# Performance work log

Hardware: AMD Instinct MI355X
Metric: run time of the kernel (lower is better)

## Reference

```python
import jax, jax.numpy as jnp
import numpy as np
import math

N_HEAD = 16

def setup_inputs() -> dict:
    key = jax.random.key(0)
    ks = jax.random.split(key, 5)
    B, T, C = 4, 2048, 2048
    s = 1.0 / math.sqrt(C)
    return {
        "x": jax.random.normal(ks[0], (B, T, C), jnp.float32),
        "w_attn": jax.random.normal(ks[1], (C, 3 * C), jnp.float32) * s,
        "b_attn": jax.random.normal(ks[2], (3 * C,), jnp.float32) * 0.01,
        "w_proj": jax.random.normal(ks[3], (C, C), jnp.float32) * s,
        "b_proj": jax.random.normal(ks[4], (C,), jnp.float32) * 0.01,
    }

def reference(x, w_attn, b_attn, w_proj, b_proj):
    B, T, C = x.shape
    H = N_HEAD
    D = C // H
    # fused QKV projection: [B,T,3C] -> [3,B,H,T,D]
    qkv = (x @ w_attn + b_attn).reshape(B, T, 3, H, D).transpose(2, 0, 3, 1, 4)
    q, k, v = qkv[0], qkv[1], qkv[2]
    scale = 1.0 / math.sqrt(D)
    scores = jnp.einsum("bhqd,bhkd->bhqk", q, k) * scale  # [B,H,T,T]
    causal = jnp.tril(jnp.ones((T, T), dtype=bool))
    neg = jnp.finfo(scores.dtype).min
    scores = jnp.where(causal, scores, neg)
    attn = jax.nn.softmax(scores, axis=-1)
    y = jnp.einsum("bhqk,bhkd->bhqd", attn, v)  # [B,H,T,D]
    y = y.transpose(0, 2, 1, 3).reshape(B, T, C)
    return y @ w_proj + b_proj
```

## Files before the change

kernel.cpp:

```cpp
#include <hip/hip_runtime.h>
#include <hip/hip_bf16.h>
#include <stdint.h>

typedef unsigned short u16;
typedef __bf16 bf16x8 __attribute__((ext_vector_type(8)));
typedef unsigned short u16x8 __attribute__((ext_vector_type(8)));
typedef float f32x4 __attribute__((ext_vector_type(4)));

__device__ __forceinline__ float bf2f(u16 u){ union{float f; unsigned i;} v; v.i = ((unsigned)u)<<16; return v.f; }
__device__ __forceinline__ u16 f2bf(float f){ union{float f; unsigned i;} v; v.f=f; unsigned r = v.i + 0x7FFFu + ((v.i>>16)&1u); return (u16)(r>>16); }

__device__ __forceinline__ void async16(const void* g, void* l){
  __builtin_amdgcn_global_load_lds((const __attribute__((address_space(1))) void*)g,
                                   (__attribute__((address_space(3))) void*)l, 16, 0, 0);
}

__global__ __launch_bounds__(256) void cvt_f2b(const float* __restrict__ src, u16* __restrict__ dst, int n)
{
  int i = (blockIdx.x * 256 + threadIdx.x) * 4;
  if (i < n) {
    float4 v = *(const float4*)&src[i];
    ushort4 o;
    o.x = f2bf(v.x); o.y = f2bf(v.y); o.z = f2bf(v.z); o.w = f2bf(v.w);
    *(ushort4*)&dst[i] = o;
  }
}

__global__ __launch_bounds__(256) void transpose2d_f2b(const float* __restrict__ src, u16* __restrict__ dst,
                                                       int src_rows, int src_cols)
{
  __shared__ u16 tile[64][72];
  const int r0 = blockIdx.y << 6, c0 = blockIdx.x << 6;
  const int t = threadIdx.x;
  #pragma unroll
  for (int i=0;i<4;i++){
    int slot = t + (i<<8);
    int r = slot >> 4, cv = (slot & 15) << 2;
    float4 v = *(const float4*)&src[(size_t)(r0+r)*src_cols + c0 + cv];
    tile[r][cv+0] = f2bf(v.x); tile[r][cv+1] = f2bf(v.y);
    tile[r][cv+2] = f2bf(v.z); tile[r][cv+3] = f2bf(v.w);
  }
  __syncthreads();
  #pragma unroll
  for (int i=0;i<2;i++){
    int slot = t + (i<<8);
    int cr = slot >> 3, rv = (slot & 7) << 3;
    u16x8 v;
    #pragma unroll
    for (int e=0;e<8;e++) v[e] = tile[rv+e][cr];
    *(u16x8*)&dst[(size_t)(c0+cr)*src_rows + r0 + rv] = v;
  }
}

__global__ __launch_bounds__(256) void transpose_v(const u16* __restrict__ qkv, u16* __restrict__ vt)
{
  __shared__ u16 tile[64][72];
  const int bh = blockIdx.z;
  const int b = bh >> 4, h = bh & 15;
  const u16* src = qkv + (size_t)b*2048*6144 + 4096 + h*128;
  u16* dst = vt + (size_t)bh*128*2048;
  const int t0 = blockIdx.y << 6, d0 = blockIdx.x << 6;
  const int t = threadIdx.x;
  #pragma unroll
  for (int i=0;i<2;i++){
    int slot = t + (i<<8);
    int r = slot >> 3, cv = (slot & 7) << 3;
    *(u16x8*)&tile[r][cv] = *(const u16x8*)&src[(size_t)(t0+r)*6144 + d0 + cv];
  }
  __syncthreads();
  #pragma unroll
  for (int i=0;i<2;i++){
    int slot = t + (i<<8);
    int cr = slot >> 3, rv = (slot & 7) << 3;
    u16x8 v;
    #pragma unroll
    for (int e=0;e<8;e++) v[e] = tile[rv+e][cr];
    *(u16x8*)&dst[(size_t)(d0+cr)*2048 + t0 + rv] = v;
  }
}

template<int F32OUT>
__global__ __launch_bounds__(512, 2) void gemm8p(const u16* __restrict__ A, const u16* __restrict__ Bt,
                                                 const float* __restrict__ bias, void* __restrict__ Cv,
                                                 int M, int N, int K, int mtiles)
{
  __shared__ u16 lsA[2][2][256*32];
  __shared__ u16 lsB[2][2][256*32];
  const int tid = threadIdx.x;
  const int w = tid >> 6, lane = tid & 63;
  const int wm = w >> 2, wn = w & 3;
  const int lo = lane & 15, hi = lane >> 4;

  const int nwg = gridDim.x;
  const int bid = blockIdx.x;
  const int swz = (bid & 7) * (nwg >> 3) + (bid >> 3);
  const int mt = swz % mtiles, nt = swz / mtiles;
  const int m0 = mt << 8, n0 = nt << 8;
  const int NT = K >> 6, NI = NT >> 1;

  const int s0 = tid, s1 = tid + 512;
  const size_t off0 = (size_t)(s0>>2)*K + (size_t)((((s0&3) ^ ((s0>>3)&3))) << 3);
  const size_t off1 = (size_t)(s1>>2)*K + (size_t)((((s1&3) ^ ((s1>>3)&3))) << 3);
  const u16* Asrc = A + (size_t)m0*K;
  const u16* Bsrc = Bt + (size_t)n0*K;

  f32x4 acc[8][4];
  f32x4 z = {0.f,0.f,0.f,0.f};
  #pragma unroll
  for (int i=0;i<8;i++)
    #pragma unroll
    for (int j=0;j<4;j++) acc[i][j] = z;

  bf16x8 bfr[4];

#define SLOT(T, KH, AP, BP) do { \
    const u16* as_ = Asrc + (T)*64 + (KH)*32; \
    const u16* bs_ = Bsrc + (T)*64 + (KH)*32; \
    async16(as_ + off0, &(AP)[s0*8]); \
    async16(as_ + off1, &(AP)[s1*8]); \
    async16(bs_ + off0, &(BP)[s0*8]); \
    async16(bs_ + off1, &(BP)[s1*8]); \
  } while(0)

#define LOADB(BUF, KS) do { \
    _Pragma("unroll") \
    for (int nf=0; nf<4; ++nf){ \
      int row_ = wn*64 + nf*16 + lo; \
      bfr[nf] = *(const bf16x8*)&lsB[BUF][KS][row_*32 + ((hi ^ ((row_>>1) & 3)) << 3)]; \
    } } while(0)

#define VM8 asm volatile("s_waitcnt vmcnt(8)" ::: "memory")
#define VM4 asm volatile("s_waitcnt vmcnt(4)" ::: "memory")
#define VM0 asm volatile("s_waitcnt vmcnt(0)" ::: "memory")
#define VMN do{}while(0)

#define PH(BUF, KS, Q, LB, WAIT, ...) do { \
    bf16x8 a_[4]; \
    _Pragma("unroll") \
    for (int mf=0; mf<4; ++mf){ \
      int row_ = wm*128 + Q*64 + mf*16 + lo; \
      a_[mf] = *(const bf16x8*)&lsA[BUF][KS][row_*32 + ((hi ^ ((row_>>1) & 3)) << 3)]; \
    } \
    if (LB) LOADB(BUF, KS); \
    __VA_ARGS__; \
    __builtin_amdgcn_s_barrier(); \
    __builtin_amdgcn_s_setprio(1); \
    _Pragma("unroll") \
    for (int mf=0; mf<4; ++mf) \
      _Pragma("unroll") \
      for (int nf=0; nf<4; ++nf) \
        acc[Q*4+mf][nf] = __builtin_amdgcn_mfma_f32_16x16x32_bf16(a_[mf], bfr[nf], acc[Q*4+mf][nf], 0,0,0); \
    __builtin_amdgcn_s_setprio(0); \
    WAIT; \
    __builtin_amdgcn_s_barrier(); \
    __builtin_amdgcn_sched_barrier(0); \
  } while(0)

  SLOT(0, 0, lsA[0][0], lsB[0][0]);
  SLOT(0, 1, lsA[0][1], lsB[0][1]);
  SLOT(1, 0, lsA[1][0], lsB[1][0]);
  VM8;
  __builtin_amdgcn_s_barrier();
  __builtin_amdgcn_sched_barrier(0);

  #pragma unroll 1
  for (int i = 0; i < NI-1; ++i){
    const int t0 = 2*i;
    PH(0,0,0, 1, VMN, SLOT(t0+1,1, lsA[1][1], lsB[1][1]));
    PH(0,0,1, 0, VM8, VMN);
    PH(0,1,0, 1, VMN, SLOT(t0+2,0, lsA[0][0], lsB[0][0]));
    PH(0,1,1, 0, VM8, VMN);
    PH(1,0,0, 1, VMN, SLOT(t0+2,1, lsA[0][1], lsB[0][1]));
    PH(1,0,1, 0, VM8, VMN);
    PH(1,1,0, 1, VMN, SLOT(t0+3,0, lsA[1][0], lsB[1][0]));
    PH(1,1,1, 0, VM8, VMN);
  }
  PH(0,0,0, 1, VMN, SLOT(NT-1,1, lsA[1][1], lsB[1][1]));
  PH(0,0,1, 0, VM8, VMN);
  PH(0,1,0, 1, VMN, VMN);
  PH(0,1,1, 0, VM4, VMN);
  PH(1,0,0, 1, VMN, VMN);
  PH(1,0,1, 0, VM0, VMN);
  PH(1,1,0, 1, VMN, VMN);
  PH(1,1,1, 0, VMN, VMN);

#undef PH
#undef SLOT
#undef LOADB

  float bv[4];
  #pragma unroll
  for (int nf=0;nf<4;nf++) bv[nf] = bias[n0 + wn*64 + nf*16 + lo];
  #pragma unroll
  for (int am=0;am<8;am++){
    int row = m0 + wm*128 + am*16 + hi*4;
    #pragma unroll
    for (int nf=0;nf<4;nf++){
      int col = n0 + wn*64 + nf*16 + lo;
      #pragma unroll
      for (int r=0;r<4;r++){
        float vv = acc[am][nf][r] + bv[nf];
        if (F32OUT) ((float*)Cv)[(size_t)(row+r)*N + col] = vv;
        else        ((u16*)Cv)[(size_t)(row+r)*N + col] = f2bf(vv);
      }
    }
  }
}

__global__ __launch_bounds__(512, 4) void attn_fwd(const u16* __restrict__ qkv, const u16* __restrict__ vt,
                                                   u16* __restrict__ y)
{
  __shared__ u16 kb[2][64*128];
  __shared__ u16 vb[2][128*64];
  __shared__ u16 plds[8][16*64];
  const int bh = blockIdx.y;
  const int b = bh >> 4, h = bh & 15;
  const int pair = blockIdx.x;
  const int tid = threadIdx.x;
  const int w = tid >> 6, lane = tid & 63;
  const int lo = lane & 15, hi = lane >> 4;

  const u16* Qb = qkv + (size_t)b*2048*6144 + h*128;
  const u16* Kb = Qb + 2048;
  const u16* Vb = vt + (size_t)bh*128*2048;
  u16* pw = &plds[w][0];
  const float sc = 0.08838834764831845f * 1.4426950408889634f;
  f32x4 z = {0.f,0.f,0.f,0.f};

  #pragma unroll 1
  for (int seg = 0; seg < 2; ++seg){
    const int qt = seg ? pair : 15 - pair;
    const int qw = qt*128 + w*16;
    const int nt = qt*2 + 2;

    bf16x8 qf[4];
    #pragma unroll
    for (int kd=0;kd<4;kd++)
      qf[kd] = *(const bf16x8*)&Qb[(size_t)(qw + lo)*6144 + kd*32 + hi*8];

    f32x4 o[8];
    #pragma unroll
    for (int dj=0;dj<8;dj++) o[dj] = z;
    float mx[4], lsum[4];
    #pragma unroll
    for (int r=0;r<4;r++){ mx[r] = -3.0e38f; lsum[r] = 0.f; }

    #pragma unroll
    for (int i=0;i<2;i++){
      int slot = i*512 + tid;
      int kr = slot >> 4;
      int kc = ((slot & 15) << 4) ^ ((kr & 7) << 4);
      async16(Kb + (size_t)kr*6144 + (kc >> 1), &kb[0][(size_t)(i*512 + w*64)*8]);
      int vr = slot >> 3;
      int vc = ((slot & 7) << 4) ^ ((vr & 7) << 4);
      async16(Vb + (size_t)vr*2048 + (vc >> 1), &vb[0][(size_t)(i*512 + w*64)*8]);
    }
    __syncthreads();

    #pragma unroll 1
    for (int it = 0; it < nt; ++it){
      const int k0 = it*64;
      if (it + 1 < nt){
        const int kn = (it+1)*64;
        u16* kdst = kb[(it+1)&1];
        u16* vdst = vb[(it+1)&1];
        #pragma unroll
        for (int i=0;i<2;i++){
          int slot = i*512 + tid;
          int kr = slot >> 4;
          int kc = ((slot & 15) << 4) ^ ((kr & 7) << 4);
          async16(Kb + (size_t)(kn + kr)*6144 + (kc >> 1), &kdst[(size_t)(i*512 + w*64)*8]);
          int vr = slot >> 3;
          int vc = ((slot & 7) << 4) ^ ((vr & 7) << 4);
          async16(Vb + (size_t)vr*2048 + kn + (vc >> 1), &vdst[(size_t)(i*512 + w*64)*8]);
        }
      }
      if (k0 <= qw + 15){
        const u16* kcur = kb[it&1];
        const u16* vcur = vb[it&1];
        f32x4 s[4];
        #pragma unroll
        for (int t=0;t<4;t++) s[t] = z;
        __builtin_amdgcn_s_setprio(1);
        #pragma unroll
        for (int t=0;t<4;t++){
          #pragma unroll
          for (int kd=0;kd<4;kd++){
            int row = t*16 + lo;
            int cb = (kd*64 + hi*16) ^ ((lo & 7) << 4);
            bf16x8 kk = *(const bf16x8*)&kcur[row*128 + (cb >> 1)];
            s[t] = __builtin_amdgcn_mfma_f32_16x16x32_bf16(qf[kd], kk, s[t], 0,0,0);
          }
        }
        __builtin_amdgcn_s_setprio(0);

        if (k0 + 63 > qw) {
          #pragma unroll
          for (int t=0;t<4;t++)
            #pragma unroll
            for (int r=0;r<4;r++){
              int q = qw + hi*4 + r;
              int k = k0 + t*16 + lo;
              if (k > q) s[t][r] = -3.0e38f;
            }
        }
        #pragma unroll
        for (int r=0;r<4;r++){
          float tm = fmaxf(fmaxf(s[0][r], s[1][r]), fmaxf(s[2][r], s[3][r]));
          tm = fmaxf(tm, __shfl_xor(tm, 1));
          tm = fmaxf(tm, __shfl_xor(tm, 2));
          tm = fmaxf(tm, __shfl_xor(tm, 4));
          tm = fmaxf(tm, __shfl_xor(tm, 8));
          tm *= sc;
          float mn = fmaxf(mx[r], tm);
          float al = exp2f(mx[r] - mn);
          mx[r] = mn;
          float p0 = exp2f(fmaf(s[0][r], sc, -mn));
          float p1 = exp2f(fmaf(s[1][r], sc, -mn));
          float p2 = exp2f(fmaf(s[2][r], sc, -mn));
          float p3 = exp2f(fmaf(s[3][r], sc, -mn));
          float sum = (p0 + p1) + (p2 + p3);
          sum += __shfl_xor(sum, 1);
          sum += __shfl_xor(sum, 2);
          sum += __shfl_xor(sum, 4);
          sum += __shfl_xor(sum, 8);
          lsum[r] = lsum[r]*al + sum;
          #pragma unroll
          for (int dj=0;dj<8;dj++) o[dj][r] *= al;
          int row = hi*4 + r;
          int sw = (row & 7) << 4;
          u16* prow = pw + row*64;
          prow[((     lo*2) ^ sw) >> 1] = f2bf(p0);
          prow[((32 + lo*2) ^ sw) >> 1] = f2bf(p1);
          prow[((64 + lo*2) ^ sw) >> 1] = f2bf(p2);
          prow[((96 + lo*2) ^ sw) >> 1] = f2bf(p3);
        }

        bf16x8 pa[2];
        #pragma unroll
        for (int kf=0;kf<2;kf++)
          pa[kf] = *(const bf16x8*)&pw[(lo*128 + ((kf*64 + hi*16) ^ ((lo & 7) << 4))) >> 1];
        __builtin_amdgcn_s_setprio(1);
        #pragma unroll
        for (int dj=0;dj<8;dj++){
          int row = dj*16 + lo;
          int cb0 = (hi*16)      ^ ((lo & 7) << 4);
          int cb1 = (64 + hi*16) ^ ((lo & 7) << 4);
          bf16x8 vv0 = *(const bf16x8*)&vcur[row*64 + (cb0 >> 1)];
          bf16x8 vv1 = *(const bf16x8*)&vcur[row*64 + (cb1 >> 1)];
          o[dj] = __builtin_amdgcn_mfma_f32_16x16x32_bf16(pa[0], vv0, o[dj], 0,0,0);
          o[dj] = __builtin_amdgcn_mfma_f32_16x16x32_bf16(pa[1], vv1, o[dj], 0,0,0);
        }
        __builtin_amdgcn_s_setprio(0);
      }
      __syncthreads();
    }

    #pragma unroll
    for (int r=0;r<4;r++){
      float inv = 1.0f / lsum[r];
      size_t row = (size_t)(b*2048 + qw + hi*4 + r);
      #pragma unroll
      for (int dj=0;dj<8;dj++)
        y[row*2048 + h*128 + dj*16 + lo] = f2bf(o[dj][r] * inv);
    }
    __syncthreads();
  }
}

extern "C" void kernel_launch(void* const* d_in, const int* in_sizes, int n_in,
                              void* d_out, int out_size, void* d_ws, size_t ws_size,
                              hipStream_t stream) {
  (void)in_sizes; (void)n_in; (void)out_size; (void)ws_size;
  const float* x      = (const float*)d_in[0];
  const float* w_attn = (const float*)d_in[1];
  const float* b_attn = (const float*)d_in[2];
  const float* w_proj = (const float*)d_in[3];
  const float* b_proj = (const float*)d_in[4];
  float* out = (float*)d_out;

  char* ws = (char*)d_ws;
  u16* xbf = (u16*)(ws);
  u16* wT  = (u16*)(ws + 33554432);
  u16* pT  = (u16*)(ws + 58720256);
  u16* qkv = (u16*)(ws + 67108864);
  u16* vt  = (u16*)(ws + 167772160);
  u16* y   = xbf;

  cvt_f2b<<<16384, 256, 0, stream>>>(x, xbf, 8192*2048);
  transpose2d_f2b<<<dim3(96,32), 256, 0, stream>>>(w_attn, wT, 2048, 6144);
  transpose2d_f2b<<<dim3(32,32), 256, 0, stream>>>(w_proj, pT, 2048, 2048);
  gemm8p<0><<<768, 512, 0, stream>>>(xbf, wT, b_attn, qkv, 8192, 6144, 2048, 32);
  transpose_v<<<dim3(2,32,64), 256, 0, stream>>>(qkv, vt);
  attn_fwd<<<dim3(8,64), 512, 0, stream>>>(qkv, vt, y);
  gemm8p<1><<<256, 512, 0, stream>>>(y, pT, b_proj, out, 8192, 2048, 2048, 32);
}
```

Measured before the change: 527.1 us.

## Software-pipeline LDS fragment reads one phase ahead of MFMA in GEMM

Restructures the GEMM main loop so LDS reads for the next phase's A and B fragments are issued before the current phase's MFMAs. Double-buffered register sets (aE/aO, bX/bY) and lgkmcnt waits replace the per-phase read-then-compute sequence, and one of the two barriers per phase is removed. The goal is to hide LDS read latency behind matrix-core work, at the cost of more VGPRs and more fragile waitcnt ordering.

Result: faster. 506.9 us (-3.8%).

```diff
diff --git a/kernel.cpp b/kernel.cpp
--- a/kernel.cpp
+++ b/kernel.cpp
@@ -111,7 +111,7 @@
     #pragma unroll
     for (int j=0;j<4;j++) acc[i][j] = z;
 
-  bf16x8 bfr[4];
+  bf16x8 aE[4], aO[4], bX[4], bY[4];
 
 #define SLOT(T, KH, AP, BP) do { \
     const u16* as_ = Asrc + (T)*64 + (KH)*32; \
@@ -122,39 +122,37 @@
     async16(bs_ + off1, &(BP)[s1*8]); \
   } while(0)
 
-#define LOADB(BUF, KS) do { \
+#define RDA(SET, BUF, KS, Q) do { \
+    _Pragma("unroll") \
+    for (int mf=0; mf<4; ++mf){ \
+      int row_ = wm*128 + (Q)*64 + mf*16 + lo; \
+      SET[mf] = *(const bf16x8*)&lsA[BUF][KS][row_*32 + ((hi ^ ((row_>>1) & 3)) << 3)]; \
+    } } while(0)
+
+#define RDB(SET, BUF, KS) do { \
     _Pragma("unroll") \
     for (int nf=0; nf<4; ++nf){ \
       int row_ = wn*64 + nf*16 + lo; \
-      bfr[nf] = *(const bf16x8*)&lsB[BUF][KS][row_*32 + ((hi ^ ((row_>>1) & 3)) << 3)]; \
+      SET[nf] = *(const bf16x8*)&lsB[BUF][KS][row_*32 + ((hi ^ ((row_>>1) & 3)) << 3)]; \
     } } while(0)
 
-#define VM8 asm volatile("s_waitcnt vmcnt(8)" ::: "memory")
-#define VM4 asm volatile("s_waitcnt vmcnt(4)" ::: "memory")
-#define VM0 asm volatile("s_waitcnt vmcnt(0)" ::: "memory")
-#define VMN do{}while(0)
-
-#define PH(BUF, KS, Q, LB, WAIT, ...) do { \
-    bf16x8 a_[4]; \
-    _Pragma("unroll") \
-    for (int mf=0; mf<4; ++mf){ \
-      int row_ = wm*128 + Q*64 + mf*16 + lo; \
-      a_[mf] = *(const bf16x8*)&lsA[BUF][KS][row_*32 + ((hi ^ ((row_>>1) & 3)) << 3)]; \
-    } \
-    if (LB) LOADB(BUF, KS); \
-    __VA_ARGS__; \
-    __builtin_amdgcn_s_barrier(); \
+#define MM(Q, AS, BS) do { \
     __builtin_amdgcn_s_setprio(1); \
     _Pragma("unroll") \
     for (int mf=0; mf<4; ++mf) \
       _Pragma("unroll") \
       for (int nf=0; nf<4; ++nf) \
-        acc[Q*4+mf][nf] = __builtin_amdgcn_mfma_f32_16x16x32_bf16(a_[mf], bfr[nf], acc[Q*4+mf][nf], 0,0,0); \
+        acc[(Q)*4+mf][nf] = __builtin_amdgcn_mfma_f32_16x16x32_bf16(AS[mf], BS[nf], acc[(Q)*4+mf][nf], 0,0,0); \
     __builtin_amdgcn_s_setprio(0); \
-    WAIT; \
-    __builtin_amdgcn_s_barrier(); \
-    __builtin_amdgcn_sched_barrier(0); \
   } while(0)
+
+#define LGK4 do { asm volatile("s_waitcnt lgkmcnt(4)" ::: "memory"); __builtin_amdgcn_sched_barrier(0); } while(0)
+#define LGK8 do { asm volatile("s_waitcnt lgkmcnt(8)" ::: "memory"); __builtin_amdgcn_sched_barrier(0); } while(0)
+#define LGK0 do { asm volatile("s_waitcnt lgkmcnt(0)" ::: "memory"); __builtin_amdgcn_sched_barrier(0); } while(0)
+#define VM8 asm volatile("s_waitcnt vmcnt(8)" ::: "memory")
+#define VM4 asm volatile("s_waitcnt vmcnt(4)" ::: "memory")
+#define VM0 asm volatile("s_waitcnt vmcnt(0)" ::: "memory")
+#define ENDP do { __builtin_amdgcn_s_barrier(); __builtin_amdgcn_sched_barrier(0); } while(0)
 
   SLOT(0, 0, lsA[0][0], lsB[0][0]);
   SLOT(0, 1, lsA[0][1], lsB[0][1]);
@@ -162,31 +160,33 @@
   VM8;
   __builtin_amdgcn_s_barrier();
   __builtin_amdgcn_sched_barrier(0);
+  RDA(aO, 0,0, 0); RDB(bX, 0,0);
 
   #pragma unroll 1
   for (int i = 0; i < NI-1; ++i){
     const int t0 = 2*i;
-    PH(0,0,0, 1, VMN, SLOT(t0+1,1, lsA[1][1], lsB[1][1]));
-    PH(0,0,1, 0, VM8, VMN);
-    PH(0,1,0, 1, VMN, SLOT(t0+2,0, lsA[0][0], lsB[0][0]));
-    PH(0,1,1, 0, VM8, VMN);
-    PH(1,0,0, 1, VMN, SLOT(t0+2,1, lsA[0][1], lsB[0][1]));
-    PH(1,0,1, 0, VM8, VMN);
-    PH(1,1,0, 1, VMN, SLOT(t0+3,0, lsA[1][0], lsB[1][0]));
-    PH(1,1,1, 0, VM8, VMN);
-  }
-  PH(0,0,0, 1, VMN, SLOT(NT-1,1, lsA[1][1], lsB[1][1]));
-  PH(0,0,1, 0, VM8, VMN);
-  PH(0,1,0, 1, VMN, VMN);
-  PH(0,1,1, 0, VM4, VMN);
-  PH(1,0,0, 1, VMN, VMN);
-  PH(1,0,1, 0, VM0, VMN);
-  PH(1,1,0, 1, VMN, VMN);
-  PH(1,1,1, 0, VMN, VMN);
-
-#undef PH
+    RDA(aE, 0,0, 1); SLOT(t0+1,1, lsA[1][1], lsB[1][1]); LGK4; MM(0, aO, bX); VM8; ENDP;
+    RDA(aO, 0,1, 0); RDB(bY, 0,1);                       LGK8; MM(1, aE, bX);      ENDP;
+    RDA(aE, 0,1, 1); SLOT(t0+2,0, lsA[0][0], lsB[0][0]); LGK4; MM(0, aO, bY); VM8; ENDP;
+    RDA(aO, 1,0, 0); RDB(bX, 1,0);                       LGK8; MM(1, aE, bY);      ENDP;
+    RDA(aE, 1,0, 1); SLOT(t0+2,1, lsA[0][1], lsB[0][1]); LGK4; MM(0, aO, bX); VM8; ENDP;
+    RDA(aO, 1,1, 0); RDB(bY, 1,1);                       LGK8; MM(1, aE, bX);      ENDP;
+    RDA(aE, 1,1, 1); SLOT(t0+3,0, lsA[1][0], lsB[1][0]); LGK4; MM(0, aO, bY); VM8; ENDP;
+    RDA(aO, 0,0, 0); RDB(bX, 0,0);                       LGK8; MM(1, aE, bY);      ENDP;
+  }
+  RDA(aE, 0,0, 1); SLOT(NT-1,1, lsA[1][1], lsB[1][1]);   LGK4; MM(0, aO, bX); VM8; ENDP;
+  RDA(aO, 0,1, 0); RDB(bY, 0,1);                         LGK8; MM(1, aE, bX);      ENDP;
+  RDA(aE, 0,1, 1);                                       LGK4; MM(0, aO, bY); VM4; ENDP;
+  RDA(aO, 1,0, 0); RDB(bX, 1,0);                         LGK8; MM(1, aE, bY);      ENDP;
+  RDA(aE, 1,0, 1);                                       LGK4; MM(0, aO, bX); VM0; ENDP;
+  RDA(aO, 1,1, 0); RDB(bY, 1,1);                         LGK8; MM(1, aE, bX);      ENDP;
+  RDA(aE, 1,1, 1);                                       LGK4; MM(0, aO, bY);      ENDP;
+                                                         LGK0; MM(1, aE, bY);
+
 #undef SLOT
-#undef LOADB
+#undef RDA
+#undef RDB
+#undef MM
 
   float bv[4];
   #pragma unroll
```
